# Kernel tuning notes

Measured on AMD Instinct MI355X. Metric: run time of the kernel, lower is better.

The kernel has to match this reference:

```python
import jax, jax.numpy as jnp
import numpy as np

EMB = 1024
DM = 64
NH = 16

def setup_inputs() -> dict:
    key = jax.random.key(0)
    ks = jax.random.split(key, 11)
    bs, slen = 2, 2048
    s = 1.0 / np.sqrt(EMB)
    inp = {
        'Q': jax.random.normal(ks[0], (bs, slen, EMB), jnp.float32),
        'K': jax.random.normal(ks[1], (bs, slen, EMB), jnp.float32),
        'V': jax.random.normal(ks[2], (bs, slen, EMB), jnp.float32),
        'Wq': jax.random.normal(ks[3], (EMB, DM * NH), jnp.float32) * s,
        'bq': jnp.zeros((DM * NH,), jnp.float32),
        'Wk': jax.random.normal(ks[4], (EMB, DM * NH), jnp.float32) * s,
        'bk': jnp.zeros((DM * NH,), jnp.float32),
        'Wv': jax.random.normal(ks[5], (EMB, DM * NH), jnp.float32) * s,
        'bv': jnp.zeros((DM * NH,), jnp.float32),
        'Wo': jax.random.normal(ks[6], (DM * NH, EMB), jnp.float32) * (1.0 / np.sqrt(DM * NH)),
        'bo': jnp.zeros((EMB,), jnp.float32),
    }
    return inp

def reference(Q, K, V, Wq, bq, Wk, bk, Wv, bv, Wo, bo):
    bs, q_len, _ = Q.shape
    kv_len = K.shape[1]
    scale = 1.0 / np.sqrt(DM)
    # project and split heads: (n, l, h, d)
    q = (scale * (Q @ Wq + bq)).reshape(bs, q_len, NH, DM)
    k = (K @ Wk + bk).reshape(bs, kv_len, NH, DM)
    v = (V @ Wv + bv).reshape(bs, kv_len, NH, DM)
    # scores (n, h, l, s) -- full S x S matrix, as in the original
    qk = jnp.einsum('nlhd,nshd->nhls', q, k)
    a = jax.nn.softmax(qk, axis=-1)  # dropout p=0 -> identity
    o = jnp.einsum('nhls,nshd->nlhd', a, v).reshape(bs, q_len, NH * DM)
    return o @ Wo + bo
```

## Files before the change

### kernel.cpp

```cpp
#include <hip/hip_runtime.h>
#include <cstdint>
#include <cstddef>

#define EMB  1024
#define DM   64
#define NH   16
#define SLEN 2048
#define BS   2

typedef _Float16 f16x8 __attribute__((ext_vector_type(8)));
typedef _Float16 f16x4 __attribute__((ext_vector_type(4)));
typedef __fp16   hf2   __attribute__((ext_vector_type(2)));
typedef __fp16   hf4   __attribute__((ext_vector_type(4)));
typedef __fp16   hf8   __attribute__((ext_vector_type(8)));
typedef float    f32x4 __attribute__((ext_vector_type(4)));

#define ASYNC_LD16(gp, lp)                                                        \
    __builtin_amdgcn_global_load_lds(                                             \
        (const __attribute__((address_space(1))) void*)(gp),                      \
        (__attribute__((address_space(3))) void*)(lp), 16, 0, 0)

__global__ __launch_bounds__(256)
void prep(const float* __restrict__ Q, const float* __restrict__ K,
          const float* __restrict__ V,
          const float* __restrict__ Wq, const float* __restrict__ Wk,
          const float* __restrict__ Wv, const float* __restrict__ Wo,
          _Float16* __restrict__ Qh, _Float16* __restrict__ Kh,
          _Float16* __restrict__ Vh,
          _Float16* __restrict__ WqT, _Float16* __restrict__ WkT,
          _Float16* __restrict__ WvT, _Float16* __restrict__ WoT)
{
    __shared__ float t[64][65];
    const int z = blockIdx.z;
    if (z < 3) {
        const float* in  = (z == 0) ? Q : (z == 1) ? K : V;
        _Float16*    out = (z == 0) ? Qh : (z == 1) ? Kh : Vh;
        size_t i = ((size_t)blockIdx.x * 256 + threadIdx.x) * 8;
        float4 a = *(const float4*)(in + i);
        float4 b = *(const float4*)(in + i + 4);
        f16x8 o;
        o[0] = (_Float16)a.x; o[1] = (_Float16)a.y; o[2] = (_Float16)a.z; o[3] = (_Float16)a.w;
        o[4] = (_Float16)b.x; o[5] = (_Float16)b.y; o[6] = (_Float16)b.z; o[7] = (_Float16)b.w;
        *(f16x8*)(out + i) = o;
        return;
    }
    if (blockIdx.x >= 256) return;
    const float* W;
    _Float16*    T;
    switch (z - 3) {
        case 0:  W = Wq; T = WqT; break;
        case 1:  W = Wk; T = WkT; break;
        case 2:  W = Wv; T = WvT; break;
        default: W = Wo; T = WoT; break;
    }
    const int tid = threadIdx.x;
    const int bn  = (blockIdx.x & 15) * 64;
    const int bk  = (blockIdx.x >> 4) * 64;

    #pragma unroll
    for (int p = 0; p < 4; ++p) {
        int row = p * 16 + (tid >> 4);
        int col = (tid & 15) * 4;
        float4 v = *(const float4*)(W + (size_t)(bk + row) * EMB + bn + col);
        t[row][col+0] = v.x; t[row][col+1] = v.y; t[row][col+2] = v.z; t[row][col+3] = v.w;
    }
    __syncthreads();
    #pragma unroll
    for (int p = 0; p < 4; ++p) {
        int nr = p * 16 + (tid >> 4);
        int kc = (tid & 15) * 4;
        f16x4 o;
        o[0] = (_Float16)t[kc+0][nr];
        o[1] = (_Float16)t[kc+1][nr];
        o[2] = (_Float16)t[kc+2][nr];
        o[3] = (_Float16)t[kc+3][nr];
        *(f16x4*)&T[(size_t)(bn + nr) * EMB + bk + kc] = o;
    }
}

__device__ __forceinline__
void gemm_core(const _Float16* __restrict__ A, const _Float16* __restrict__ Bt,
               const float* __restrict__ bias, float* __restrict__ Cf,
               _Float16* __restrict__ Ch, int M, int N, int K,
               float scale, int mode, int bx, int by)
{
    __shared__ __align__(16) _Float16 As[64 * 64];
    __shared__ __align__(16) _Float16 Bs[128 * 64];

    const int tid  = threadIdx.x;
    const int lane = tid & 63;
    const int wave = tid >> 6;
    const int c    = lane & 15;
    const int quad = lane >> 4;
    const int bm   = by * 64;
    const int bn   = bx * 128;
    const int wm   = (wave >> 1) * 32;
    const int wn   = (wave & 1) * 64;

    f32x4 acc[2][4];
    #pragma unroll
    for (int i = 0; i < 2; ++i)
        #pragma unroll
        for (int j = 0; j < 4; ++j)
            #pragma unroll
            for (int r = 0; r < 4; ++r) acc[i][j][r] = 0.f;

    const size_t Kb = (size_t)K * 2;
    const int    lc = ((tid & 7) ^ ((tid >> 3) & 7)) * 16;
    const char* gA = (const char*)A  + (size_t)(bm + (tid >> 3)) * Kb + lc;
    const char* gB = (const char*)Bt + (size_t)(bn + (tid >> 3)) * Kb + lc;
    char* lA = (char*)As + wave * 1024;
    char* lB = (char*)Bs + wave * 1024;

    for (int k0 = 0; k0 < K; k0 += 64) {
        const size_t ko = (size_t)k0 * 2;
        __syncthreads();
        ASYNC_LD16(gA + ko,           lA);
        ASYNC_LD16(gA + 32*Kb + ko,   lA + 4096);
        ASYNC_LD16(gB + ko,           lB);
        ASYNC_LD16(gB + 32*Kb + ko,   lB + 4096);
        ASYNC_LD16(gB + 64*Kb + ko,   lB + 8192);
        ASYNC_LD16(gB + 96*Kb + ko,   lB + 12288);
        __syncthreads();

        #pragma unroll
        for (int kk = 0; kk < 2; ++kk) {
            f16x8 af[2], bf[4];
            #pragma unroll
            for (int i = 0; i < 2; ++i)
                af[i] = *(const f16x8*)
                    &As[(wm + i*16 + c) * 64 + (((kk*4 + quad) ^ (c & 7)) * 8)];
            #pragma unroll
            for (int j = 0; j < 4; ++j)
                bf[j] = *(const f16x8*)
                    &Bs[(wn + j*16 + c) * 64 + (((kk*4 + quad) ^ (c & 7)) * 8)];
            #pragma unroll
            for (int i = 0; i < 2; ++i)
                #pragma unroll
                for (int j = 0; j < 4; ++j)
                    acc[i][j] = __builtin_amdgcn_mfma_f32_16x16x32_f16(af[i], bf[j], acc[i][j], 0, 0, 0);
        }
    }

    float bcol[4];
    #pragma unroll
    for (int j = 0; j < 4; ++j) bcol[j] = bias[bn + wn + j * 16 + c];

    #pragma unroll
    for (int i = 0; i < 2; ++i) {
        int m0 = bm + wm + i * 16 + quad * 4;
        #pragma unroll
        for (int j = 0; j < 4; ++j) {
            int n = bn + wn + j * 16 + c;
            if (mode == 0) {
                #pragma unroll
                for (int r = 0; r < 4; ++r)
                    Cf[(size_t)(m0 + r) * N + n] = acc[i][j][r] + bcol[j];
            } else if (mode == 1) {
                int h = n >> 6, d = n & 63;
                #pragma unroll
                for (int r = 0; r < 4; ++r) {
                    int mm = m0 + r;
                    int b = mm >> 11, l = mm & (SLEN - 1);
                    Ch[(((size_t)(b * NH + h)) * SLEN + l) * DM + d] =
                        (_Float16)((acc[i][j][r] + bcol[j]) * scale);
                }
            } else {
                int h = n >> 6, d = n & 63;
                int b = m0 >> 11, l = m0 & (SLEN - 1);
                f16x4 o;
                #pragma unroll
                for (int r = 0; r < 4; ++r)
                    o[r] = (_Float16)(acc[i][j][r] + bcol[j]);
                *(f16x4*)&Ch[(((size_t)(b * NH + h)) * DM + d) * SLEN + l] = o;
            }
        }
    }
}

__global__ __launch_bounds__(256)
void gemm_qkv(const _Float16* __restrict__ Qh, const _Float16* __restrict__ Kh,
              const _Float16* __restrict__ Vh,
              const _Float16* __restrict__ WqT, const _Float16* __restrict__ WkT,
              const _Float16* __restrict__ WvT,
              const float* __restrict__ bq, const float* __restrict__ bk,
              const float* __restrict__ bv,
              _Float16* __restrict__ q_ws, _Float16* __restrict__ k_ws,
              _Float16* __restrict__ v_ws)
{
    const _Float16 *A, *Bt;
    const float* bias;
    _Float16* Ch;
    float scale;
    int mode;
    if (blockIdx.z == 0)      { A = Qh; Bt = WqT; bias = bq; Ch = q_ws; scale = 0.18033688f; mode = 1; }
    else if (blockIdx.z == 1) { A = Kh; Bt = WkT; bias = bk; Ch = k_ws; scale = 1.0f;        mode = 1; }
    else                      { A = Vh; Bt = WvT; bias = bv; Ch = v_ws; scale = 1.0f;        mode = 2; }
    gemm_core(A, Bt, bias, nullptr, Ch, BS * SLEN, NH * DM, EMB, scale, mode,
              blockIdx.x, blockIdx.y);
}

__global__ __launch_bounds__(256)
void gemm_out(const _Float16* __restrict__ Oh, const _Float16* __restrict__ WoT,
              const float* __restrict__ bo, float* __restrict__ out)
{
    gemm_core(Oh, WoT, bo, out, nullptr, BS * SLEN, EMB, NH * DM, 1.0f, 0,
              blockIdx.x, blockIdx.y);
}

__global__ __launch_bounds__(512)
void attn_mfma(const _Float16* __restrict__ qw, const _Float16* __restrict__ kw,
               const _Float16* __restrict__ vwT, _Float16* __restrict__ ow)
{
    __shared__ __align__(16) _Float16 Kt[2][64 * 64];
    __shared__ __align__(16) _Float16 Vt[2][64 * 64];

    const int tid  = threadIdx.x;
    const int lane = tid & 63;
    const int wave = tid >> 6;
    const int c    = lane & 15;
    const int quad = lane >> 4;
    const int qg   = wave & 3;
    const int kh   = wave >> 2;
    const int bh   = blockIdx.y;
    const int b    = bh >> 4;
    const int h    = bh & 15;
    const int qbase = blockIdx.x * 128 + qg * 32;

    const _Float16* kb = kw  + (size_t)bh * SLEN * DM;
    const _Float16* vb = vwT + (size_t)bh * DM * SLEN;
    const _Float16* qb = qw  + (size_t)bh * SLEN * DM;

    f16x8 qf[2][2];
    #pragma unroll
    for (int t = 0; t < 2; ++t)
        #pragma unroll
        for (int ch = 0; ch < 2; ++ch)
            qf[t][ch] = *(const f16x8*)(qb + (size_t)(qbase + t*16 + c) * DM + ch*32 + quad*8);

    f32x4 oacc[2][4];
    f32x4 lacc[2];
    #pragma unroll
    for (int t = 0; t < 2; ++t) {
        #pragma unroll
        for (int dg = 0; dg < 4; ++dg)
            #pragma unroll
            for (int r = 0; r < 4; ++r) oacc[t][dg][r] = 0.f;
        #pragma unroll
        for (int r = 0; r < 4; ++r) lacc[t][r] = 0.f;
    }

    const f16x8 ones8 = {(_Float16)1.f, (_Float16)1.f, (_Float16)1.f, (_Float16)1.f,
                         (_Float16)1.f, (_Float16)1.f, (_Float16)1.f, (_Float16)1.f};
    const f32x4 zero4 = {0.f, 0.f, 0.f, 0.f};

    const int r0  = wave * 8 + (lane >> 3);
    const int lc0 = (((lane & 7) ^ ((lane >> 3) & 7)) * 16);
    const char* gk = (const char*)kb + r0 * 128 + lc0;
    const char* gv = (const char*)vb + (size_t)r0 * 4096 + lc0;
    char* lK = (char*)&Kt[0][0] + wave * 1024;
    char* lV = (char*)&Vt[0][0] + wave * 1024;

    ASYNC_LD16(gk, lK);
    ASYNC_LD16(gv, lV);
    gk += 8192; gv += 128;
    __syncthreads();

    auto tile = [&](int cur, bool pf) {
        if (pf) {
            char* pk = (char*)&Kt[cur ^ 1][0] + wave * 1024;
            char* pv = (char*)&Vt[cur ^ 1][0] + wave * 1024;
            ASYNC_LD16(gk, pk);
            ASYNC_LD16(gv, pv);
            gk += 8192; gv += 128;
        }

        f16x8 kf[2][2];
        #pragma unroll
        for (int kg = 0; kg < 2; ++kg)
            #pragma unroll
            for (int ch = 0; ch < 2; ++ch)
                kf[kg][ch] = *(const f16x8*)
                    &Kt[cur][(kh*32 + kg*16 + c) * 64 + (((ch*4 + quad) ^ (c & 7)) * 8)];

        f32x4 s[2][2];
        #pragma unroll
        for (int t = 0; t < 2; ++t)
            #pragma unroll
            for (int kg = 0; kg < 2; ++kg) {
                s[t][kg] = __builtin_amdgcn_mfma_f32_16x16x32_f16(kf[kg][0], qf[t][0], zero4,   0, 0, 0);
                s[t][kg] = __builtin_amdgcn_mfma_f32_16x16x32_f16(kf[kg][1], qf[t][1], s[t][kg], 0, 0, 0);
            }

        f16x8 pf8[2];
        #pragma unroll
        for (int t = 0; t < 2; ++t) {
            hf4 h4[2];
            #pragma unroll
            for (int u = 0; u < 2; ++u) {
                float p0 = __builtin_amdgcn_exp2f(s[t][u][0]);
                float p1 = __builtin_amdgcn_exp2f(s[t][u][1]);
                float p2 = __builtin_amdgcn_exp2f(s[t][u][2]);
                float p3 = __builtin_amdgcn_exp2f(s[t][u][3]);
                hf2 lo = __builtin_amdgcn_cvt_pkrtz(p0, p1);
                hf2 hi = __builtin_amdgcn_cvt_pkrtz(p2, p3);
                h4[u] = __builtin_shufflevector(lo, hi, 0, 1, 2, 3);
            }
            hf8 h8 = __builtin_shufflevector(h4[0], h4[1], 0, 1, 2, 3, 4, 5, 6, 7);
            pf8[t] = __builtin_bit_cast(f16x8, h8);
        }

        #pragma unroll
        for (int t = 0; t < 2; ++t)
            lacc[t] = __builtin_amdgcn_mfma_f32_16x16x32_f16(pf8[t], ones8, lacc[t], 0, 0, 0);

        #pragma unroll
        for (int dg = 0; dg < 4; ++dg) {
            f16x4 vf[2];
            #pragma unroll
            for (int u = 0; u < 2; ++u)
                vf[u] = *(const f16x4*)
                    &Vt[cur][(dg*16 + c) * 64 +
                             (((kh*4 + 2*u + (quad >> 1)) ^ (c & 7)) * 8) + (quad & 1) * 4];
            f16x8 v8 = __builtin_shufflevector(vf[0], vf[1], 0, 1, 2, 3, 4, 5, 6, 7);
            #pragma unroll
            for (int t = 0; t < 2; ++t)
                oacc[t][dg] = __builtin_amdgcn_mfma_f32_16x16x32_f16(pf8[t], v8, oacc[t][dg], 0, 0, 0);
        }
        __syncthreads();
    };

    for (int it = 0; it < SLEN / 64 - 2; it += 2) {
        tile(0, true);
        tile(1, true);
    }
    tile(0, true);
    tile(1, false);

    float* mb = (float*)&Kt[0][0];
    #pragma unroll
    for (int t = 0; t < 2; ++t) {
        if (kh == 1) {
            float* p = mb + ((qg * 64 + lane) * 20);
            *(f32x4*)(p +  0) = oacc[t][0];
            *(f32x4*)(p +  4) = oacc[t][1];
            *(f32x4*)(p +  8) = oacc[t][2];
            *(f32x4*)(p + 12) = oacc[t][3];
            *(f32x4*)(p + 16) = lacc[t];
        }
        __syncthreads();
        if (kh == 0) {
            const float* p = mb + ((qg * 64 + lane) * 20);
            f32x4 po[4], pl;
            po[0] = *(const f32x4*)(p +  0);
            po[1] = *(const f32x4*)(p +  4);
            po[2] = *(const f32x4*)(p +  8);
            po[3] = *(const f32x4*)(p + 12);
            pl    = *(const f32x4*)(p + 16);
            #pragma unroll
            for (int r = 0; r < 4; ++r) {
                float linv = 1.0f / (lacc[t][r] + pl[r]);
                int row = qbase + t*16 + quad*4 + r;
                #pragma unroll
                for (int dg = 0; dg < 4; ++dg)
                    ow[((size_t)b * SLEN + row) * EMB + h * DM + dg*16 + c] =
                        (_Float16)((oacc[t][dg][r] + po[dg][r]) * linv);
            }
        }
        __syncthreads();
    }
}

extern "C" void kernel_launch(void* const* d_in, const int* in_sizes, int n_in,
                              void* d_out, int out_size, void* d_ws, size_t ws_size,
                              hipStream_t stream)
{
    const float* Q  = (const float*)d_in[0];
    const float* K  = (const float*)d_in[1];
    const float* V  = (const float*)d_in[2];
    const float* Wq = (const float*)d_in[3];
    const float* bq = (const float*)d_in[4];
    const float* Wk = (const float*)d_in[5];
    const float* bk = (const float*)d_in[6];
    const float* Wv = (const float*)d_in[7];
    const float* bv = (const float*)d_in[8];
    const float* Wo = (const float*)d_in[9];
    const float* bo = (const float*)d_in[10];
    float* out = (float*)d_out;

    const size_t MN = (size_t)BS * SLEN * NH * DM;
    const size_t WW = (size_t)EMB * NH * DM;

    _Float16* base = (_Float16*)d_ws;
    _Float16* Qh   = base;
    _Float16* Kh   = Qh  + MN;
    _Float16* Vh   = Kh  + MN;
    _Float16* WqT  = Vh  + MN;
    _Float16* WkT  = WqT + WW;
    _Float16* WvT  = WkT + WW;
    _Float16* WoT  = WvT + WW;
    _Float16* q_ws = WoT + WW;
    _Float16* k_ws = q_ws + MN;
    _Float16* v_ws = k_ws + MN;
    _Float16* o_ws = v_ws + MN;

    dim3 blk(256);

    prep<<<dim3(2048, 1, 7), blk, 0, stream>>>(Q, K, V, Wq, Wk, Wv, Wo,
                                               Qh, Kh, Vh, WqT, WkT, WvT, WoT);

    gemm_qkv<<<dim3(8, 64, 3), blk, 0, stream>>>(Qh, Kh, Vh, WqT, WkT, WvT,
                                                 bq, bk, bv, q_ws, k_ws, v_ws);

    attn_mfma<<<dim3(SLEN / 128, BS * NH), dim3(512), 0, stream>>>(q_ws, k_ws, v_ws, o_ws);

    gemm_out<<<dim3(8, 64, 1), blk, 0, stream>>>(o_ws, WoT, bo, out);
}
```

Baseline: 226.0 us.

## Double-buffer GEMM LDS tiles and swizzle block indices for XCD locality

The shared GEMM core now uses two LDS buffers, so the asynchronous global-to-LDS loads for the next K tile are issued before the MFMA work on the current tile. This removes one barrier per iteration and is meant to hide global load latency. Both GEMM kernels also remap block indices so that consecutive workgroups share the same B (weight) column tile, aiming for better L2 reuse within an XCD. The cost is doubled LDS use, which may lower occupancy, and the remap assumes a fixed 8x64 grid shape.

```diff
diff --git a/kernel.cpp b/kernel.cpp
--- a/kernel.cpp
+++ b/kernel.cpp
@@ -84,8 +84,8 @@
                _Float16* __restrict__ Ch, int M, int N, int K,
                float scale, int mode, int bx, int by)
 {
-    __shared__ __align__(16) _Float16 As[64 * 64];
-    __shared__ __align__(16) _Float16 Bs[128 * 64];
+    __shared__ __align__(16) _Float16 As[2][64 * 64];
+    __shared__ __align__(16) _Float16 Bs[2][128 * 64];
 
     const int tid  = threadIdx.x;
     const int lane = tid & 63;
@@ -109,19 +109,27 @@
     const int    lc = ((tid & 7) ^ ((tid >> 3) & 7)) * 16;
     const char* gA = (const char*)A  + (size_t)(bm + (tid >> 3)) * Kb + lc;
     const char* gB = (const char*)Bt + (size_t)(bn + (tid >> 3)) * Kb + lc;
-    char* lA = (char*)As + wave * 1024;
-    char* lB = (char*)Bs + wave * 1024;
-
-    for (int k0 = 0; k0 < K; k0 += 64) {
-        const size_t ko = (size_t)k0 * 2;
-        __syncthreads();
+
+    const int NS = K / 64;
+
+    auto stage = [&](int buf, int t) {
+        const size_t ko = (size_t)t * 128;
+        char* lA = (char*)&As[buf][0] + wave * 1024;
+        char* lB = (char*)&Bs[buf][0] + wave * 1024;
         ASYNC_LD16(gA + ko,           lA);
         ASYNC_LD16(gA + 32*Kb + ko,   lA + 4096);
         ASYNC_LD16(gB + ko,           lB);
         ASYNC_LD16(gB + 32*Kb + ko,   lB + 4096);
         ASYNC_LD16(gB + 64*Kb + ko,   lB + 8192);
         ASYNC_LD16(gB + 96*Kb + ko,   lB + 12288);
-        __syncthreads();
+    };
+
+    stage(0, 0);
+    __syncthreads();
+
+    int cur = 0;
+    for (int t = 0; t < NS; ++t) {
+        if (t + 1 < NS) stage(cur ^ 1, t + 1);
 
         #pragma unroll
         for (int kk = 0; kk < 2; ++kk) {
@@ -129,17 +137,19 @@
             #pragma unroll
             for (int i = 0; i < 2; ++i)
                 af[i] = *(const f16x8*)
-                    &As[(wm + i*16 + c) * 64 + (((kk*4 + quad) ^ (c & 7)) * 8)];
+                    &As[cur][(wm + i*16 + c) * 64 + (((kk*4 + quad) ^ (c & 7)) * 8)];
             #pragma unroll
             for (int j = 0; j < 4; ++j)
                 bf[j] = *(const f16x8*)
-                    &Bs[(wn + j*16 + c) * 64 + (((kk*4 + quad) ^ (c & 7)) * 8)];
+                    &Bs[cur][(wn + j*16 + c) * 64 + (((kk*4 + quad) ^ (c & 7)) * 8)];
             #pragma unroll
             for (int i = 0; i < 2; ++i)
                 #pragma unroll
                 for (int j = 0; j < 4; ++j)
                     acc[i][j] = __builtin_amdgcn_mfma_f32_16x16x32_f16(af[i], bf[j], acc[i][j], 0, 0, 0);
         }
+        __syncthreads();
+        cur ^= 1;
     }
 
     float bcol[4];
@@ -178,6 +188,13 @@
     }
 }
 
+__device__ __forceinline__ void xcd_swz(int& bx, int& by)
+{
+    int wid = blockIdx.x + 8 * blockIdx.y;
+    bx = wid >> 6;
+    by = wid & 63;
+}
+
 __global__ __launch_bounds__(256)
 void gemm_qkv(const _Float16* __restrict__ Qh, const _Float16* __restrict__ Kh,
               const _Float16* __restrict__ Vh,
@@ -196,16 +213,16 @@
     if (blockIdx.z == 0)      { A = Qh; Bt = WqT; bias = bq; Ch = q_ws; scale = 0.18033688f; mode = 1; }
     else if (blockIdx.z == 1) { A = Kh; Bt = WkT; bias = bk; Ch = k_ws; scale = 1.0f;        mode = 1; }
     else                      { A = Vh; Bt = WvT; bias = bv; Ch = v_ws; scale = 1.0f;        mode = 2; }
-    gemm_core(A, Bt, bias, nullptr, Ch, BS * SLEN, NH * DM, EMB, scale, mode,
-              blockIdx.x, blockIdx.y);
+    int bx, by; xcd_swz(bx, by);
+    gemm_core(A, Bt, bias, nullptr, Ch, BS * SLEN, NH * DM, EMB, scale, mode, bx, by);
 }
 
 __global__ __launch_bounds__(256)
 void gemm_out(const _Float16* __restrict__ Oh, const _Float16* __restrict__ WoT,
               const float* __restrict__ bo, float* __restrict__ out)
 {
-    gemm_core(Oh, WoT, bo, out, nullptr, BS * SLEN, EMB, NH * DM, 1.0f, 0,
-              blockIdx.x, blockIdx.y);
+    int bx, by; xcd_swz(bx, by);
+    gemm_core(Oh, WoT, bo, out, nullptr, BS * SLEN, EMB, NH * DM, 1.0f, 0, bx, by);
 }
 
 __global__ __launch_bounds__(512)
```

Measured after the change: 218.6 us. 1.03x faster.
